# Performance work log

Measured on AMD Instinct MI355X. Metric: run time of the kernel, lower is better.

The kernel has to match this reference:

```python
import jax, jax.numpy as jnp
import numpy as np

B, IN, OUT, K = 2048, 1024, 1024, 20


def setup_inputs() -> dict:
    key = jax.random.key(0)
    k1, k2 = jax.random.split(key)
    x = jax.random.normal(k1, (B, IN), dtype=jnp.float32)
    # per-output, per-input spline coefficients: (out_features, in_features, num_knots)
    W = jax.random.normal(k2, (OUT, IN, K), dtype=jnp.float32) * 0.1
    # evenly spaced knot grid on [-2, 2] (linspace)
    knots = jnp.linspace(-2.0, 2.0, K, dtype=jnp.float32)
    return {"x": x, "W": W, "knots": knots}


def reference(x, W, knots):
    # RBF spline basis shared across all output features (this is the fusion
    # the original per-output Python loop misses):
    # basis[b, i, k] = exp(-0.5 * ((x[b, i] - knots[k]) / h)^2)
    h = knots[1] - knots[0]  # uniform knot spacing -> RBF bandwidth
    basis = jnp.exp(-0.5 * jnp.square((x[:, :, None] - knots) / h))  # (B, IN, K)
    # Each SplineLayer o computes sum_{i,k} W[o,i,k] * basis[b,i,k]; the
    # KANBlock concatenates the OUT scalars -> a single einsum.
    return jnp.einsum("bik,oik->bo", basis, W)  # (B, OUT)
```

## Files before the change

kernel.cpp:

```cpp
#include <hip/hip_runtime.h>

#define B_DIM 2048
#define IN_DIM 1024
#define OUT_DIM 1024
#define K_KNOTS 20
#define KR (IN_DIM * K_KNOTS)
#define OUT_ELEMS (B_DIM * OUT_DIM)
#define KS 8

#define NPAIRS (B_DIM * IN_DIM * 5 / 2)
#define NB_BASIS_BLK (NPAIRS / 256)
#define NW4 (OUT_DIM * KR / 8)
#define NB_W_BLK (NW4 / 256)

typedef __bf16 bf16x8 __attribute__((ext_vector_type(8)));
typedef float  f32x4  __attribute__((ext_vector_type(4)));

#define MFMA16(a, b, c) __builtin_amdgcn_mfma_f32_16x16x32_bf16(a, b, c, 0, 0, 0)

__device__ __forceinline__ unsigned short f2bf(float f) {
    unsigned int u = __float_as_uint(f);
    unsigned int r = u + 0x7fffu + ((u >> 16) & 1u);
    return (unsigned short)(r >> 16);
}

__device__ __forceinline__ unsigned int pack2(float lo, float hi) {
    return (unsigned int)f2bf(lo) | ((unsigned int)f2bf(hi) << 16);
}

__device__ __forceinline__ void async_load16(const void* g, void* l) {
    __builtin_amdgcn_global_load_lds(
        (const __attribute__((address_space(1))) void*)g,
        (__attribute__((address_space(3))) void*)l,
        16, 0, 0);
}

__global__ void __launch_bounds__(256) prep_kernel(
        const float* __restrict__ x,
        const float4* __restrict__ Wsrc,
        const float* __restrict__ knots,
        uint4* __restrict__ basis_out,
        uint4* __restrict__ w_out) {
    if (blockIdx.x < NB_BASIS_BLK) {
        const unsigned int p  = blockIdx.x * 256 + threadIdx.x;
        const unsigned int n0 = 2 * p;
        const unsigned int q0  = n0 % 5u;
        const unsigned int bi0 = n0 / 5u;
        const float t0   = knots[0];
        const float h    = knots[1] - t0;
        const float invh = 1.0f / h;

        const bool cross = (q0 == 4u);
        const unsigned int bi1 = bi0 + (cross ? 1u : 0u);
        const float xv0 = x[bi0];
        const float xv1 = x[bi1];
        const float kA = (float)(4u * q0);
        const float kB = cross ? 0.f : kA + 4.f;

        float v[8];
#pragma unroll
        for (int j = 0; j < 4; ++j) {
            float t = __builtin_fmaf(kA + (float)j, h, t0);
            float d = (xv0 - t) * invh;
            v[j] = __expf(-0.5f * d * d);
        }
#pragma unroll
        for (int j = 0; j < 4; ++j) {
            float t = __builtin_fmaf(kB + (float)j, h, t0);
            float d = (xv1 - t) * invh;
            v[4 + j] = __expf(-0.5f * d * d);
        }
        uint4 o;
        o.x = pack2(v[0], v[1]); o.y = pack2(v[2], v[3]);
        o.z = pack2(v[4], v[5]); o.w = pack2(v[6], v[7]);
        basis_out[p] = o;
    } else {
        unsigned int t = (blockIdx.x - NB_BASIS_BLK) * 256 + threadIdx.x;
        float4 a = Wsrc[2 * t];
        float4 b = Wsrc[2 * t + 1];
        uint4 o;
        o.x = pack2(a.x, a.y);
        o.y = pack2(a.z, a.w);
        o.z = pack2(b.x, b.y);
        o.w = pack2(b.z, b.w);
        w_out[t] = o;
    }
}

#define AOFF(s, h) (((s) * 2 + (h)) * 8192)
#define BOFF(s, h) (32768 + ((s) * 2 + (h)) * 8192)

template <int S>
__device__ __forceinline__ void tile_step(
        int t, int ntiles,
        const unsigned short* __restrict__ Ab,
        const unsigned short* __restrict__ Bb,
        unsigned short* lds,
        f32x4 (&acc)[8][4],
        int m0, int n0, int k0,
        int wave, int wm, int wn, int r15, int c0, int c1,
        int srow8, int scol) {
    const int aB  = S * 16384 + (wm * 128 + r15) * 64;
    const int bB  = 32768 + S * 16384 + (wn * 64 + r15) * 64;
    const int kb1 = k0 + (t + 1) * 64;
    const bool st = (t + 1 < ntiles);

    auto stage = [&](const unsigned short* __restrict__ src, int grow, int kb, int lbase) {
        const unsigned short* g = src + (size_t)(grow + wave * 16 + srow8) * KR + kb + scol;
        async_load16(g,                  &lds[lbase + wave * 1024]);
        async_load16(g + (size_t)8 * KR, &lds[lbase + wave * 1024 + 512]);
    };

    bf16x8 a0[4], a1[4], b0[4], b1[4], s0[4], s1[4];

#pragma unroll
    for (int i = 0; i < 4; ++i) a0[i] = *(const bf16x8*)&lds[aB + i * 1024 + c0];
#pragma unroll
    for (int j = 0; j < 4; ++j) b0[j] = *(const bf16x8*)&lds[bB + j * 1024 + c0];
    __builtin_amdgcn_s_barrier();
    asm volatile("s_waitcnt lgkmcnt(0)" ::: "memory");
    __builtin_amdgcn_sched_barrier(0);
    __builtin_amdgcn_s_setprio(1);
#pragma unroll
    for (int i = 0; i < 4; ++i)
#pragma unroll
        for (int j = 0; j < 4; ++j)
            acc[i][j] = MFMA16(a0[i], b0[j], acc[i][j]);
    __builtin_amdgcn_s_setprio(0);

#pragma unroll
    for (int i = 0; i < 4; ++i) a1[i] = *(const bf16x8*)&lds[aB + i * 1024 + c1];
#pragma unroll
    for (int j = 0; j < 4; ++j) b1[j] = *(const bf16x8*)&lds[bB + j * 1024 + c1];
    __builtin_amdgcn_s_barrier();
    asm volatile("s_waitcnt lgkmcnt(0)" ::: "memory");
    __builtin_amdgcn_sched_barrier(0);
    __builtin_amdgcn_s_setprio(1);
#pragma unroll
    for (int i = 0; i < 4; ++i)
#pragma unroll
        for (int j = 0; j < 4; ++j)
            acc[i][j] = MFMA16(a1[i], b1[j], acc[i][j]);
    __builtin_amdgcn_s_setprio(0);

#pragma unroll
    for (int i = 0; i < 4; ++i) s0[i] = *(const bf16x8*)&lds[aB + (4 + i) * 1024 + c0];
    if (st) {
        stage(Ab, m0,       kb1, AOFF(S ^ 1, 0));
        stage(Ab, m0 + 128, kb1, AOFF(S ^ 1, 1));
    }
    __builtin_amdgcn_s_barrier();
    asm volatile("s_waitcnt lgkmcnt(0)" ::: "memory");
    __builtin_amdgcn_sched_barrier(0);
    __builtin_amdgcn_s_setprio(1);
#pragma unroll
    for (int i = 0; i < 4; ++i)
#pragma unroll
        for (int j = 0; j < 4; ++j)
            acc[4 + i][j] = MFMA16(s0[i], b0[j], acc[4 + i][j]);
    __builtin_amdgcn_s_setprio(0);

#pragma unroll
    for (int i = 0; i < 4; ++i) s1[i] = *(const bf16x8*)&lds[aB + (4 + i) * 1024 + c1];
    if (st) {
        stage(Bb, n0,       kb1, BOFF(S ^ 1, 0));
        stage(Bb, n0 + 128, kb1, BOFF(S ^ 1, 1));
    }
    __builtin_amdgcn_s_barrier();
    asm volatile("s_waitcnt lgkmcnt(0)" ::: "memory");
    __builtin_amdgcn_sched_barrier(0);
    __builtin_amdgcn_s_setprio(1);
#pragma unroll
    for (int i = 0; i < 4; ++i)
#pragma unroll
        for (int j = 0; j < 4; ++j)
            acc[4 + i][j] = MFMA16(s1[i], b1[j], acc[4 + i][j]);
    __builtin_amdgcn_s_setprio(0);

    if (st) asm volatile("s_waitcnt vmcnt(0)" ::: "memory");
    __builtin_amdgcn_s_barrier();
}

__global__ void __launch_bounds__(512, 2)
kan_gemm8(const unsigned short* __restrict__ Ab,
          const unsigned short* __restrict__ Bb,
          float* __restrict__ part) {
    __shared__ __align__(16) unsigned short lds[65536];

    constexpr int KPBk   = KR / KS;
    constexpr int NTILES = KPBk / 64;

    const int id  = blockIdx.x;
    const int z   = id & 7;
    const int ord = id >> 3;
    const int mt  = ord & 7;
    const int nt  = ord >> 3;
    const int m0  = mt * 256;
    const int n0  = nt * 256;
    const int k0  = z * KPBk;

    const int tid  = threadIdx.x;
    const int wave = tid >> 6;
    const int lane = tid & 63;
    const int wm   = wave >> 2;
    const int wn   = wave & 3;

    const int srow8 = lane >> 3;
    const int scol  = ((lane & 7) ^ srow8) * 8;

    auto stage = [&](const unsigned short* __restrict__ src, int grow, int kb, int lbase) {
        const unsigned short* g = src + (size_t)(grow + wave * 16 + srow8) * KR + kb + scol;
        async_load16(g,                  &lds[lbase + wave * 1024]);
        async_load16(g + (size_t)8 * KR, &lds[lbase + wave * 1024 + 512]);
    };

    f32x4 acc[8][4];
#pragma unroll
    for (int i = 0; i < 8; ++i)
#pragma unroll
        for (int j = 0; j < 4; ++j) acc[i][j] = (f32x4){0.f, 0.f, 0.f, 0.f};

    const int q   = lane >> 4;
    const int r15 = lane & 15;
    const int r7  = lane & 7;
    const int c0  = (q ^ r7) * 8;
    const int c1  = ((4 + q) ^ r7) * 8;

    stage(Ab, m0,       k0, AOFF(0, 0));
    stage(Ab, m0 + 128, k0, AOFF(0, 1));
    stage(Bb, n0,       k0, BOFF(0, 0));
    stage(Bb, n0 + 128, k0, BOFF(0, 1));
    asm volatile("s_waitcnt vmcnt(0)" ::: "memory");
    __builtin_amdgcn_s_barrier();

    for (int tt = 0; tt < NTILES; tt += 2) {
        tile_step<0>(tt,     NTILES, Ab, Bb, lds, acc, m0, n0, k0,
                     wave, wm, wn, r15, c0, c1, srow8, scol);
        tile_step<1>(tt + 1, NTILES, Ab, Bb, lds, acc, m0, n0, k0,
                     wave, wm, wn, r15, c0, c1, srow8, scol);
    }

    float* dst = part + (size_t)z * OUT_ELEMS;
#pragma unroll
    for (int i = 0; i < 8; ++i)
#pragma unroll
        for (int j = 0; j < 4; ++j)
#pragma unroll
            for (int r = 0; r < 4; ++r) {
                const int row = m0 + wm * 128 + i * 16 + q * 4 + r;
                const int c   = n0 + wn * 64  + j * 16 + r15;
                dst[(size_t)row * OUT_DIM + c] = acc[i][j][r];
            }
}

template <int KSr>
__global__ void kan_reduce(const float* __restrict__ part, float* __restrict__ out) {
    const int idx = (blockIdx.x * 256 + threadIdx.x) * 4;
    f32x4 s = *(const f32x4*)(part + idx);
#pragma unroll
    for (int z = 1; z < KSr; ++z)
        s += *(const f32x4*)(part + (size_t)z * OUT_ELEMS + idx);
    *(f32x4*)(out + idx) = s;
}

__global__ void kan_fallback(const float* __restrict__ x,
                             const float* __restrict__ W,
                             const float* __restrict__ knots,
                             float* __restrict__ out) {
    __shared__ float basis[256 * K_KNOTS];
    const int b = blockIdx.x;
    const int o = blockIdx.y * blockDim.x + threadIdx.x;
    const float invh = 1.0f / (knots[1] - knots[0]);
    const float* w = W + (size_t)o * KR;
    float sum = 0.f;
    for (int i0 = 0; i0 < IN_DIM; i0 += 256) {
        __syncthreads();
        for (int idx = threadIdx.x; idx < 256 * K_KNOTS; idx += blockDim.x) {
            const int i = i0 + idx / K_KNOTS;
            const int k = idx % K_KNOTS;
            const float d = (x[(size_t)b * IN_DIM + i] - knots[k]) * invh;
            basis[idx] = __expf(-0.5f * d * d);
        }
        __syncthreads();
        for (int r = 0; r < 256 * K_KNOTS; ++r)
            sum += basis[r] * w[(size_t)i0 * K_KNOTS + r];
    }
    out[(size_t)b * OUT_DIM + o] = sum;
}

extern "C" void kernel_launch(void* const* d_in, const int* in_sizes, int n_in,
                              void* d_out, int out_size, void* d_ws, size_t ws_size,
                              hipStream_t stream) {
    const float* x     = (const float*)d_in[0];
    const float* W     = (const float*)d_in[1];
    const float* knots = (const float*)d_in[2];
    float* out = (float*)d_out;

    const size_t basis_bytes = (size_t)B_DIM * KR * 2;
    const size_t wb_bytes    = (size_t)OUT_DIM * KR * 2;
    const size_t part_bytes  = (size_t)KS * OUT_ELEMS * 4;

    unsigned short* Ab = (unsigned short*)d_ws;
    unsigned short* Bb = (unsigned short*)((char*)d_ws + basis_bytes);
    float* part = (float*)((char*)d_ws + basis_bytes + wb_bytes);

    if (ws_size >= basis_bytes + wb_bytes + part_bytes) {
        prep_kernel<<<dim3(NB_BASIS_BLK + NB_W_BLK), dim3(256), 0, stream>>>(
            x, (const float4*)W, knots, (uint4*)Ab, (uint4*)Bb);
        kan_gemm8<<<dim3(256), dim3(512), 0, stream>>>(Ab, Bb, part);
        kan_reduce<KS><<<dim3(OUT_ELEMS / (256 * 4)), dim3(256), 0, stream>>>(part, out);
    } else {
        kan_fallback<<<dim3(B_DIM, OUT_DIM / 256), dim3(256), 0, stream>>>(x, W, knots, out);
    }
}
```

Measured before the change: 246.2 us.

## Split LDS tiles by K-half and issue finer-grained async prefetches with partial waits

The LDS layout changes from 256-row by 64-K tiles with 8-way XOR swizzle to two K-halves of 32 columns each, with a 4-way swizzle. Loads for the next tile are issued per K-half spread across the four MFMA phases. Partial vmcnt waits (vmcnt(2), vmcnt(4)) replace the full drain plus trailing barrier at the end of each step. The aim is to overlap global-to-LDS traffic with MFMA work and remove one barrier per tile. In exchange, correctness now depends on exact counts of in-flight loads, and the narrower swizzle may raise LDS bank conflicts.

```diff
diff --git a/kernel.cpp b/kernel.cpp
--- a/kernel.cpp
+++ b/kernel.cpp
@@ -87,8 +87,8 @@
     }
 }
 
-#define AOFF(s, h) (((s) * 2 + (h)) * 8192)
-#define BOFF(s, h) (32768 + ((s) * 2 + (h)) * 8192)
+#define AOF(s, kh) (((s) * 2 + (kh)) * 8192)
+#define BOF(s, kh) (32768 + ((s) * 2 + (kh)) * 8192)
 
 template <int S>
 __device__ __forceinline__ void tile_step(
@@ -98,25 +98,26 @@
         unsigned short* lds,
         f32x4 (&acc)[8][4],
         int m0, int n0, int k0,
-        int wave, int wm, int wn, int r15, int c0, int c1,
-        int srow8, int scol) {
-    const int aB  = S * 16384 + (wm * 128 + r15) * 64;
-    const int bB  = 32768 + S * 16384 + (wn * 64 + r15) * 64;
+        int wave, int rowA, int rowB,
+        int srow32, int scol32) {
     const int kb1 = k0 + (t + 1) * 64;
     const bool st = (t + 1 < ntiles);
 
-    auto stage = [&](const unsigned short* __restrict__ src, int grow, int kb, int lbase) {
-        const unsigned short* g = src + (size_t)(grow + wave * 16 + srow8) * KR + kb + scol;
-        async_load16(g,                  &lds[lbase + wave * 1024]);
-        async_load16(g + (size_t)8 * KR, &lds[lbase + wave * 1024 + 512]);
+    auto stage_half = [&](const unsigned short* __restrict__ src, int grow,
+                          int kc, int lbase) {
+        const unsigned short* g =
+            src + (size_t)(grow + wave * 32 + srow32) * KR + kc + scol32;
+        async_load16(g,                   &lds[lbase + wave * 1024]);
+        async_load16(g + (size_t)16 * KR, &lds[lbase + wave * 1024 + 512]);
     };
 
     bf16x8 a0[4], a1[4], b0[4], b1[4], s0[4], s1[4];
 
 #pragma unroll
-    for (int i = 0; i < 4; ++i) a0[i] = *(const bf16x8*)&lds[aB + i * 1024 + c0];
-#pragma unroll
-    for (int j = 0; j < 4; ++j) b0[j] = *(const bf16x8*)&lds[bB + j * 1024 + c0];
+    for (int i = 0; i < 4; ++i) a0[i] = *(const bf16x8*)&lds[AOF(S, 0) + rowA + i * 512];
+#pragma unroll
+    for (int j = 0; j < 4; ++j) b0[j] = *(const bf16x8*)&lds[BOF(S, 0) + rowB + j * 512];
+    if (st) stage_half(Ab, m0, kb1, AOF(S ^ 1, 0));
     __builtin_amdgcn_s_barrier();
     asm volatile("s_waitcnt lgkmcnt(0)" ::: "memory");
     __builtin_amdgcn_sched_barrier(0);
@@ -128,10 +129,13 @@
             acc[i][j] = MFMA16(a0[i], b0[j], acc[i][j]);
     __builtin_amdgcn_s_setprio(0);
 
-#pragma unroll
-    for (int i = 0; i < 4; ++i) a1[i] = *(const bf16x8*)&lds[aB + i * 1024 + c1];
-#pragma unroll
-    for (int j = 0; j < 4; ++j) b1[j] = *(const bf16x8*)&lds[bB + j * 1024 + c1];
+    if (st) asm volatile("s_waitcnt vmcnt(2)" ::: "memory");
+    else    asm volatile("s_waitcnt vmcnt(0)" ::: "memory");
+#pragma unroll
+    for (int i = 0; i < 4; ++i) a1[i] = *(const bf16x8*)&lds[AOF(S, 1) + rowA + i * 512];
+#pragma unroll
+    for (int j = 0; j < 4; ++j) b1[j] = *(const bf16x8*)&lds[BOF(S, 1) + rowB + j * 512];
+    if (st) stage_half(Bb, n0, kb1, BOF(S ^ 1, 0));
     __builtin_amdgcn_s_barrier();
     asm volatile("s_waitcnt lgkmcnt(0)" ::: "memory");
     __builtin_amdgcn_sched_barrier(0);
@@ -144,11 +148,8 @@
     __builtin_amdgcn_s_setprio(0);
 
 #pragma unroll
-    for (int i = 0; i < 4; ++i) s0[i] = *(const bf16x8*)&lds[aB + (4 + i) * 1024 + c0];
-    if (st) {
-        stage(Ab, m0,       kb1, AOFF(S ^ 1, 0));
-        stage(Ab, m0 + 128, kb1, AOFF(S ^ 1, 1));
-    }
+    for (int i = 0; i < 4; ++i) s0[i] = *(const bf16x8*)&lds[AOF(S, 0) + rowA + (4 + i) * 512];
+    if (st) stage_half(Ab, m0, kb1 + 32, AOF(S ^ 1, 1));
     __builtin_amdgcn_s_barrier();
     asm volatile("s_waitcnt lgkmcnt(0)" ::: "memory");
     __builtin_amdgcn_sched_barrier(0);
@@ -161,10 +162,10 @@
     __builtin_amdgcn_s_setprio(0);
 
 #pragma unroll
-    for (int i = 0; i < 4; ++i) s1[i] = *(const bf16x8*)&lds[aB + (4 + i) * 1024 + c1];
+    for (int i = 0; i < 4; ++i) s1[i] = *(const bf16x8*)&lds[AOF(S, 1) + rowA + (4 + i) * 512];
     if (st) {
-        stage(Bb, n0,       kb1, BOFF(S ^ 1, 0));
-        stage(Bb, n0 + 128, kb1, BOFF(S ^ 1, 1));
+        stage_half(Bb, n0, kb1 + 32, BOF(S ^ 1, 1));
+        asm volatile("s_waitcnt vmcnt(4)" ::: "memory");
     }
     __builtin_amdgcn_s_barrier();
     asm volatile("s_waitcnt lgkmcnt(0)" ::: "memory");
@@ -176,9 +177,6 @@
         for (int j = 0; j < 4; ++j)
             acc[4 + i][j] = MFMA16(s1[i], b1[j], acc[4 + i][j]);
     __builtin_amdgcn_s_setprio(0);
-
-    if (st) asm volatile("s_waitcnt vmcnt(0)" ::: "memory");
-    __builtin_amdgcn_s_barrier();
 }
 
 __global__ void __launch_bounds__(512, 2)
@@ -205,13 +203,15 @@
     const int wm   = wave >> 2;
     const int wn   = wave & 3;
 
-    const int srow8 = lane >> 3;
-    const int scol  = ((lane & 7) ^ srow8) * 8;
-
-    auto stage = [&](const unsigned short* __restrict__ src, int grow, int kb, int lbase) {
-        const unsigned short* g = src + (size_t)(grow + wave * 16 + srow8) * KR + kb + scol;
-        async_load16(g,                  &lds[lbase + wave * 1024]);
-        async_load16(g + (size_t)8 * KR, &lds[lbase + wave * 1024 + 512]);
+    const int srow32 = lane >> 2;
+    const int scol32 = ((lane & 3) ^ (srow32 & 3)) * 8;
+
+    auto stage_half = [&](const unsigned short* __restrict__ src, int grow,
+                          int kc, int lbase) {
+        const unsigned short* g =
+            src + (size_t)(grow + wave * 32 + srow32) * KR + kc + scol32;
+        async_load16(g,                   &lds[lbase + wave * 1024]);
+        async_load16(g + (size_t)16 * KR, &lds[lbase + wave * 1024 + 512]);
     };
 
     f32x4 acc[8][4];
@@ -220,24 +220,24 @@
 #pragma unroll
         for (int j = 0; j < 4; ++j) acc[i][j] = (f32x4){0.f, 0.f, 0.f, 0.f};
 
-    const int q   = lane >> 4;
-    const int r15 = lane & 15;
-    const int r7  = lane & 7;
-    const int c0  = (q ^ r7) * 8;
-    const int c1  = ((4 + q) ^ r7) * 8;
-
-    stage(Ab, m0,       k0, AOFF(0, 0));
-    stage(Ab, m0 + 128, k0, AOFF(0, 1));
-    stage(Bb, n0,       k0, BOFF(0, 0));
-    stage(Bb, n0 + 128, k0, BOFF(0, 1));
-    asm volatile("s_waitcnt vmcnt(0)" ::: "memory");
+    const int q    = lane >> 4;
+    const int r15  = lane & 15;
+    const int cs   = (q ^ (r15 & 3)) * 8;
+    const int rowA = (wm * 128 + r15) * 32 + cs;
+    const int rowB = (wn * 64 + r15) * 32 + cs;
+
+    stage_half(Ab, m0, k0,      AOF(0, 0));
+    stage_half(Bb, n0, k0,      BOF(0, 0));
+    stage_half(Ab, m0, k0 + 32, AOF(0, 1));
+    stage_half(Bb, n0, k0 + 32, BOF(0, 1));
+    asm volatile("s_waitcnt vmcnt(4)" ::: "memory");
     __builtin_amdgcn_s_barrier();
 
     for (int tt = 0; tt < NTILES; tt += 2) {
         tile_step<0>(tt,     NTILES, Ab, Bb, lds, acc, m0, n0, k0,
-                     wave, wm, wn, r15, c0, c1, srow8, scol);
+                     wave, rowA, rowB, srow32, scol32);
         tile_step<1>(tt + 1, NTILES, Ab, Bb, lds, acc, m0, n0, k0,
-                     wave, wm, wn, r15, c0, c1, srow8, scol);
+                     wave, rowA, rowB, srow32, scol32);
     }
 
     float* dst = part + (size_t)z * OUT_ELEMS;
```

Measured after the change: 248.5 us. About the same (+0.9%).
